# Kernel optimization log

Hardware: AMD Instinct MI355X
Metric: run time of the kernel (lower is better)

The kernel has to match this reference:

```python
import jax, jax.numpy as jnp
import numpy as np

IN_CH = 16
OUT_CH = 32
INIT_LS = 0.1


def setup_inputs() -> dict:
    key = jax.random.key(0)
    k1, k2, k3, k4 = jax.random.split(key, 4)
    b, n, m = 8, 1024, 1024
    x = jax.random.normal(k1, (b, n, 1), dtype=jnp.float32)
    y = jax.random.normal(k2, (b, n, IN_CH), dtype=jnp.float32)
    t = jax.random.normal(k3, (b, m, 1), dtype=jnp.float32)
    # xavier_normal for Linear(in=16, out=32): std = sqrt(2/(fan_in+fan_out))
    std = float(np.sqrt(2.0 / (IN_CH + OUT_CH)))
    W = jax.random.normal(k4, (OUT_CH, IN_CH), dtype=jnp.float32) * std
    bias = jnp.zeros((OUT_CH,), dtype=jnp.float32)
    sigma = jnp.full((IN_CH,), np.log(INIT_LS), dtype=jnp.float32)
    return {"x": x, "y": y, "t": t, "sigma": sigma, "W": W, "bias": bias}


def reference(x, y, t, sigma, W, bias):
    # pairwise squared distances: (b, n, m)
    dists = (x - jnp.transpose(t, (0, 2, 1))) ** 2
    scales = jnp.exp(sigma)  # (C,)
    # RBF weights per channel: (b, n, m, C)
    wt = jnp.exp(-0.5 * dists[..., None] / (scales ** 2))
    # weighted sum over observations n -> (b, m, C)
    y_out = jnp.einsum('bnmc,bnc->bmc', wt, y)
    # pointwise linear: (b, m, out_channels)
    return jnp.einsum('bmc,oc->bmo', y_out, W) + bias
```

## Files before the change

kernel.cpp:

```cpp
#include <hip/hip_runtime.h>


#define B_SZ 8
#define N_SZ 1024
#define M_SZ 1024
#define C_SZ 16
#define O_SZ 32
#define LOG2E 1.4426950408889634f

typedef _Float16 f16x8 __attribute__((ext_vector_type(8)));
typedef __fp16   h16x2 __attribute__((ext_vector_type(2)));
typedef float    f32x4 __attribute__((ext_vector_type(4)));

__global__ __launch_bounds__(512, 4) void setconv_fused(
    const float* __restrict__ x,
    const float* __restrict__ y,
    const float* __restrict__ t,
    const float* __restrict__ sigma,
    const float* __restrict__ W,
    const float* __restrict__ bias,
    float* __restrict__ out)
{
    const int tid  = threadIdx.x;
    const int w    = tid >> 6;
    const int lane = tid & 63;
    const int b    = blockIdx.x >> 6;
    const int mg   = blockIdx.x & 63;

    const int g  = lane >> 4;
    const int g4 = 4 * g;
    const int c  = lane & 15;

    __shared__ float red[8][16][16];

    const float* ybc = y + ((size_t)b * N_SZ + w * 128) * C_SZ + c;
    float yraw[32];
#pragma unroll
    for (int kc = 0; kc < 4; ++kc) {
#pragma unroll
        for (int jj = 0; jj < 4; ++jj) {
            yraw[kc * 8 + jj]     = ybc[(kc * 32 + g4 + jj) * C_SZ];
            yraw[kc * 8 + 4 + jj] = ybc[(kc * 32 + 16 + g4 + jj) * C_SZ];
        }
    }
    const float* xw = x + b * N_SZ + w * 128;
    f32x4 xlo[4], xhi[4];
#pragma unroll
    for (int kc = 0; kc < 4; ++kc) {
        xlo[kc] = *(const f32x4*)(xw + kc * 32 + g4);
        xhi[kc] = *(const f32x4*)(xw + kc * 32 + 16 + g4);
    }
    const float tm = t[b * M_SZ + mg * 16 + c];
    f32x4 s0 = *(const f32x4*)(sigma + 0);
    f32x4 s1 = *(const f32x4*)(sigma + 4);
    f32x4 s2 = *(const f32x4*)(sigma + 8);
    f32x4 s3 = *(const f32x4*)(sigma + 12);

    const bool uni =
        (s0[0]==s0[1]) && (s0[0]==s0[2]) && (s0[0]==s0[3]) &&
        (s0[0]==s1[0]) && (s0[0]==s1[1]) && (s0[0]==s1[2]) && (s0[0]==s1[3]) &&
        (s0[0]==s2[0]) && (s0[0]==s2[1]) && (s0[0]==s2[2]) && (s0[0]==s2[3]) &&
        (s0[0]==s3[0]) && (s0[0]==s3[1]) && (s0[0]==s3[2]) && (s0[0]==s3[3]);

    f16x8 bf[4];
#pragma unroll
    for (int kc = 0; kc < 4; ++kc)
#pragma unroll
        for (int j = 0; j < 8; ++j)
            bf[kc][j] = (_Float16)yraw[kc * 8 + j];

    if (uni) {
        const float kcu = -0.5f * LOG2E * __builtin_amdgcn_exp2f(-2.0f * LOG2E * s0[0]);
        const float su  = __builtin_sqrtf(-kcu);
        const float nst = -su * tm;

        f32x4 acc = {0.f, 0.f, 0.f, 0.f};

#pragma unroll
        for (int kc = 0; kc < 4; ++kc) {
            float e[8];
#pragma unroll
            for (int j = 0; j < 4; ++j) {
                const float u = fmaf(su, xlo[kc][j], nst);
                e[j] = __builtin_amdgcn_exp2f(-u * u);
            }
#pragma unroll
            for (int j = 0; j < 4; ++j) {
                const float u = fmaf(su, xhi[kc][j], nst);
                e[4 + j] = __builtin_amdgcn_exp2f(-u * u);
            }
            union { h16x2 p2[4]; f16x8 v8; } au;
            au.p2[0] = __builtin_amdgcn_cvt_pkrtz(e[0], e[1]);
            au.p2[1] = __builtin_amdgcn_cvt_pkrtz(e[2], e[3]);
            au.p2[2] = __builtin_amdgcn_cvt_pkrtz(e[4], e[5]);
            au.p2[3] = __builtin_amdgcn_cvt_pkrtz(e[6], e[7]);
            acc = __builtin_amdgcn_mfma_f32_16x16x32_f16(au.v8, bf[kc], acc, 0, 0, 0);
        }

#pragma unroll
        for (int r = 0; r < 4; ++r)
            red[w][g * 4 + r][c] = acc[r];
        __syncthreads();

        if (tid < 256) {
            const int mi = tid >> 4, cc = tid & 15;
            float s = red[0][mi][cc];
#pragma unroll
            for (int wv = 1; wv < 8; ++wv) s += red[wv][mi][cc];
            red[0][mi][cc] = s;
        }
        __syncthreads();

        {
            const int mi = tid >> 5, o = tid & 31;
            const float* gr = &red[0][mi][0];
            const float* wr = W + o * C_SZ;
            float v = bias[o];
#pragma unroll
            for (int cc = 0; cc < C_SZ; ++cc) v = fmaf(gr[cc], wr[cc], v);
            out[((size_t)(b * M_SZ + mg * 16 + mi)) * O_SZ + o] = v;
        }
    } else {
        const int j  = lane >> 2;
        const int cg = lane & 3;
        f32x4 slv = *(const f32x4*)(sigma + cg * 4);
        f32x4 kl;
#pragma unroll
        for (int cc = 0; cc < 4; ++cc)
            kl[cc] = -0.5f * LOG2E * __builtin_amdgcn_exp2f(-2.0f * LOG2E * slv[cc]);

        const float tv0 = t[b * M_SZ + mg * 16 + w * 2 + 0];
        const float tv1 = t[b * M_SZ + mg * 16 + w * 2 + 1];

        f32x4 acc0 = {0.f, 0.f, 0.f, 0.f};
        f32x4 acc1 = {0.f, 0.f, 0.f, 0.f};

        for (int it = 0; it < 64; ++it) {
            const int n = it * 16 + j;
            const float xc = x[b * N_SZ + n];
            const f32x4 yc = *(const f32x4*)(y + ((size_t)b * N_SZ + n) * C_SZ + cg * 4);
            const float d0 = xc - tv0, d1 = xc - tv1;
            const float q0 = d0 * d0,  q1 = d1 * d1;
#pragma unroll
            for (int cc = 0; cc < 4; ++cc) {
                acc0[cc] = fmaf(__builtin_amdgcn_exp2f(q0 * kl[cc]), yc[cc], acc0[cc]);
                acc1[cc] = fmaf(__builtin_amdgcn_exp2f(q1 * kl[cc]), yc[cc], acc1[cc]);
            }
        }
#pragma unroll
        for (int mask = 4; mask <= 32; mask <<= 1) {
#pragma unroll
            for (int cc = 0; cc < 4; ++cc) {
                acc0[cc] += __shfl_xor(acc0[cc], mask);
                acc1[cc] += __shfl_xor(acc1[cc], mask);
            }
        }
        float* rp = &red[0][0][0];
        if (lane < 4) {
            *(f32x4*)(rp + (w * 2 + 0) * 16 + lane * 4) = acc0;
            *(f32x4*)(rp + (w * 2 + 1) * 16 + lane * 4) = acc1;
        }
        __syncthreads();
        {
            const int mi = tid >> 5, o = tid & 31;
            const float* wr = W + o * C_SZ;
            float v = bias[o];
#pragma unroll
            for (int cc = 0; cc < C_SZ; ++cc) v = fmaf(rp[mi * 16 + cc], wr[cc], v);
            out[((size_t)(b * M_SZ + mg * 16 + mi)) * O_SZ + o] = v;
        }
    }
}

extern "C" void kernel_launch(void* const* d_in, const int* in_sizes, int n_in,
                              void* d_out, int out_size, void* d_ws, size_t ws_size,
                              hipStream_t stream) {
    const float* x     = (const float*)d_in[0];
    const float* y     = (const float*)d_in[1];
    const float* t     = (const float*)d_in[2];
    const float* sigma = (const float*)d_in[3];
    const float* W     = (const float*)d_in[4];
    const float* bias  = (const float*)d_in[5];
    float* out = (float*)d_out;

    setconv_fused<<<B_SZ * 64, 512, 0, stream>>>(x, y, t, sigma, W, bias, out);
}
```

Measured before the change: 10.15 us.

## Process 32 target points per block to reuse loaded y/x fragments

Each block now handles 32 target points instead of 16, computing two MFMA accumulators that share the same fp16 y fragments and x registers. The grid halves to 256 blocks, with the batch index placed in the low bits of the block index, and launch bounds relax to 2 blocks per CU. This amortizes the per-block load of y, x and sigma and the reduction overhead over twice the outputs. The cost is fewer blocks, which may leave CUs underused on a 256-CU part, plus higher register pressure.

```diff
diff --git a/kernel.cpp b/kernel.cpp
--- a/kernel.cpp
+++ b/kernel.cpp
@@ -12,7 +12,7 @@
 typedef __fp16   h16x2 __attribute__((ext_vector_type(2)));
 typedef float    f32x4 __attribute__((ext_vector_type(4)));
 
-__global__ __launch_bounds__(512, 4) void setconv_fused(
+__global__ __launch_bounds__(512, 2) void setconv_fused(
     const float* __restrict__ x,
     const float* __restrict__ y,
     const float* __restrict__ t,
@@ -24,14 +24,14 @@
     const int tid  = threadIdx.x;
     const int w    = tid >> 6;
     const int lane = tid & 63;
-    const int b    = blockIdx.x >> 6;
-    const int mg   = blockIdx.x & 63;
+    const int b  = blockIdx.x & 7;
+    const int mg = blockIdx.x >> 3;
 
     const int g  = lane >> 4;
     const int g4 = 4 * g;
     const int c  = lane & 15;
 
-    __shared__ float red[8][16][16];
+    __shared__ float red[8][32][16];
 
     const float* ybc = y + ((size_t)b * N_SZ + w * 128) * C_SZ + c;
     float yraw[32];
@@ -50,7 +50,8 @@
         xlo[kc] = *(const f32x4*)(xw + kc * 32 + g4);
         xhi[kc] = *(const f32x4*)(xw + kc * 32 + 16 + g4);
     }
-    const float tm = t[b * M_SZ + mg * 16 + c];
+    const float tm0 = t[b * M_SZ + mg * 32 + c];
+    const float tm1 = t[b * M_SZ + mg * 32 + 16 + c];
     f32x4 s0 = *(const f32x4*)(sigma + 0);
     f32x4 s1 = *(const f32x4*)(sigma + 4);
     f32x4 s2 = *(const f32x4*)(sigma + 8);
@@ -70,39 +71,46 @@
             bf[kc][j] = (_Float16)yraw[kc * 8 + j];
 
     if (uni) {
-        const float kcu = -0.5f * LOG2E * __builtin_amdgcn_exp2f(-2.0f * LOG2E * s0[0]);
-        const float su  = __builtin_sqrtf(-kcu);
-        const float nst = -su * tm;
-
-        f32x4 acc = {0.f, 0.f, 0.f, 0.f};
+        const float kcu  = -0.5f * LOG2E * __builtin_amdgcn_exp2f(-2.0f * LOG2E * s0[0]);
+        const float su   = __builtin_sqrtf(-kcu);
+        const float nst0 = -su * tm0;
+        const float nst1 = -su * tm1;
+
+        f32x4 acc0 = {0.f, 0.f, 0.f, 0.f};
+        f32x4 acc1 = {0.f, 0.f, 0.f, 0.f};
 
 #pragma unroll
         for (int kc = 0; kc < 4; ++kc) {
-            float e[8];
+            float e0[8], e1[8];
 #pragma unroll
             for (int j = 0; j < 4; ++j) {
-                const float u = fmaf(su, xlo[kc][j], nst);
-                e[j] = __builtin_amdgcn_exp2f(-u * u);
+                const float u0 = fmaf(su, xlo[kc][j], nst0);
+                const float v0 = fmaf(su, xhi[kc][j], nst0);
+                const float u1 = fmaf(su, xlo[kc][j], nst1);
+                const float v1 = fmaf(su, xhi[kc][j], nst1);
+                e0[j]     = __builtin_amdgcn_exp2f(-u0 * u0);
+                e0[4 + j] = __builtin_amdgcn_exp2f(-v0 * v0);
+                e1[j]     = __builtin_amdgcn_exp2f(-u1 * u1);
+                e1[4 + j] = __builtin_amdgcn_exp2f(-v1 * v1);
             }
-#pragma unroll
-            for (int j = 0; j < 4; ++j) {
-                const float u = fmaf(su, xhi[kc][j], nst);
-                e[4 + j] = __builtin_amdgcn_exp2f(-u * u);
+            union { h16x2 p2[4]; f16x8 v8; } a0, a1;
+#pragma unroll
+            for (int p = 0; p < 4; ++p) {
+                a0.p2[p] = __builtin_amdgcn_cvt_pkrtz(e0[2 * p], e0[2 * p + 1]);
+                a1.p2[p] = __builtin_amdgcn_cvt_pkrtz(e1[2 * p], e1[2 * p + 1]);
             }
-            union { h16x2 p2[4]; f16x8 v8; } au;
-            au.p2[0] = __builtin_amdgcn_cvt_pkrtz(e[0], e[1]);
-            au.p2[1] = __builtin_amdgcn_cvt_pkrtz(e[2], e[3]);
-            au.p2[2] = __builtin_amdgcn_cvt_pkrtz(e[4], e[5]);
-            au.p2[3] = __builtin_amdgcn_cvt_pkrtz(e[6], e[7]);
-            acc = __builtin_amdgcn_mfma_f32_16x16x32_f16(au.v8, bf[kc], acc, 0, 0, 0);
-        }
-
-#pragma unroll
-        for (int r = 0; r < 4; ++r)
-            red[w][g * 4 + r][c] = acc[r];
+            acc0 = __builtin_amdgcn_mfma_f32_16x16x32_f16(a0.v8, bf[kc], acc0, 0, 0, 0);
+            acc1 = __builtin_amdgcn_mfma_f32_16x16x32_f16(a1.v8, bf[kc], acc1, 0, 0, 0);
+        }
+
+#pragma unroll
+        for (int r = 0; r < 4; ++r) {
+            red[w][g * 4 + r][c]      = acc0[r];
+            red[w][16 + g * 4 + r][c] = acc1[r];
+        }
         __syncthreads();
 
-        if (tid < 256) {
+        {
             const int mi = tid >> 4, cc = tid & 15;
             float s = red[0][mi][cc];
 #pragma unroll
@@ -111,14 +119,16 @@
         }
         __syncthreads();
 
-        {
-            const int mi = tid >> 5, o = tid & 31;
+#pragma unroll
+        for (int u = 0; u < 2; ++u) {
+            const int idx = tid + u * 512;
+            const int mi = idx >> 5, o = idx & 31;
             const float* gr = &red[0][mi][0];
             const float* wr = W + o * C_SZ;
             float v = bias[o];
 #pragma unroll
             for (int cc = 0; cc < C_SZ; ++cc) v = fmaf(gr[cc], wr[cc], v);
-            out[((size_t)(b * M_SZ + mg * 16 + mi)) * O_SZ + o] = v;
+            out[((size_t)(b * M_SZ + mg * 32 + mi)) * O_SZ + o] = v;
         }
     } else {
         const int j  = lane >> 2;
@@ -129,45 +139,52 @@
         for (int cc = 0; cc < 4; ++cc)
             kl[cc] = -0.5f * LOG2E * __builtin_amdgcn_exp2f(-2.0f * LOG2E * slv[cc]);
 
-        const float tv0 = t[b * M_SZ + mg * 16 + w * 2 + 0];
-        const float tv1 = t[b * M_SZ + mg * 16 + w * 2 + 1];
-
-        f32x4 acc0 = {0.f, 0.f, 0.f, 0.f};
-        f32x4 acc1 = {0.f, 0.f, 0.f, 0.f};
+        float tv[4];
+#pragma unroll
+        for (int mm = 0; mm < 4; ++mm)
+            tv[mm] = t[b * M_SZ + mg * 32 + w * 4 + mm];
+
+        f32x4 acc[4];
+#pragma unroll
+        for (int mm = 0; mm < 4; ++mm) acc[mm] = (f32x4){0.f, 0.f, 0.f, 0.f};
 
         for (int it = 0; it < 64; ++it) {
             const int n = it * 16 + j;
             const float xc = x[b * N_SZ + n];
             const f32x4 yc = *(const f32x4*)(y + ((size_t)b * N_SZ + n) * C_SZ + cg * 4);
-            const float d0 = xc - tv0, d1 = xc - tv1;
-            const float q0 = d0 * d0,  q1 = d1 * d1;
-#pragma unroll
-            for (int cc = 0; cc < 4; ++cc) {
-                acc0[cc] = fmaf(__builtin_amdgcn_exp2f(q0 * kl[cc]), yc[cc], acc0[cc]);
-                acc1[cc] = fmaf(__builtin_amdgcn_exp2f(q1 * kl[cc]), yc[cc], acc1[cc]);
+#pragma unroll
+            for (int mm = 0; mm < 4; ++mm) {
+                const float d = xc - tv[mm];
+                const float q = d * d;
+#pragma unroll
+                for (int cc = 0; cc < 4; ++cc)
+                    acc[mm][cc] = fmaf(__builtin_amdgcn_exp2f(q * kl[cc]), yc[cc], acc[mm][cc]);
             }
         }
 #pragma unroll
-        for (int mask = 4; mask <= 32; mask <<= 1) {
-#pragma unroll
-            for (int cc = 0; cc < 4; ++cc) {
-                acc0[cc] += __shfl_xor(acc0[cc], mask);
-                acc1[cc] += __shfl_xor(acc1[cc], mask);
-            }
-        }
+        for (int mm = 0; mm < 4; ++mm)
+#pragma unroll
+            for (int mask = 4; mask <= 32; mask <<= 1)
+#pragma unroll
+                for (int cc = 0; cc < 4; ++cc)
+                    acc[mm][cc] += __shfl_xor(acc[mm][cc], mask);
+
         float* rp = &red[0][0][0];
         if (lane < 4) {
-            *(f32x4*)(rp + (w * 2 + 0) * 16 + lane * 4) = acc0;
-            *(f32x4*)(rp + (w * 2 + 1) * 16 + lane * 4) = acc1;
+#pragma unroll
+            for (int mm = 0; mm < 4; ++mm)
+                *(f32x4*)(rp + (w * 4 + mm) * 16 + lane * 4) = acc[mm];
         }
         __syncthreads();
-        {
-            const int mi = tid >> 5, o = tid & 31;
+#pragma unroll
+        for (int u = 0; u < 2; ++u) {
+            const int idx = tid + u * 512;
+            const int mi = idx >> 5, o = idx & 31;
             const float* wr = W + o * C_SZ;
             float v = bias[o];
 #pragma unroll
             for (int cc = 0; cc < C_SZ; ++cc) v = fmaf(rp[mi * 16 + cc], wr[cc], v);
-            out[((size_t)(b * M_SZ + mg * 16 + mi)) * O_SZ + o] = v;
+            out[((size_t)(b * M_SZ + mg * 32 + mi)) * O_SZ + o] = v;
         }
     }
 }
@@ -183,5 +200,5 @@
     const float* bias  = (const float*)d_in[5];
     float* out = (float*)d_out;
 
-    setconv_fused<<<B_SZ * 64, 512, 0, stream>>>(x, y, t, sigma, W, bias, out);
+    setconv_fused<<<256, 512, 0, stream>>>(x, y, t, sigma, W, bias, out);
 }
```

Result: faster. 9.688 us (-4.5%).
